# Performance work log

Measured on AMD Instinct MI355X. Metric: run time of the kernel, lower is better.

## Reference

```python
import jax, jax.numpy as jnp
import numpy as np

B, S, D, H = 2, 2048, 2048, 16
HD = D // H


def setup_inputs() -> dict:
    key = jax.random.key(0)
    ks = jax.random.split(key, 11)
    scale = 1.0 / np.sqrt(D)
    return {
        "query": jax.random.normal(ks[0], (B, S, D), jnp.float32),
        "key_": jax.random.normal(ks[1], (B, S, D), jnp.float32),
        "value": jax.random.normal(ks[2], (B, S, D), jnp.float32),
        "Wq": jax.random.normal(ks[3], (D, D), jnp.float32) * scale,
        "bq": jnp.zeros((D,), jnp.float32),
        "Wk": jax.random.normal(ks[4], (D, D), jnp.float32) * scale,
        "bk": jnp.zeros((D,), jnp.float32),
        "Wv": jax.random.normal(ks[5], (D, D), jnp.float32) * scale,
        "bv": jnp.zeros((D,), jnp.float32),
        "Wo": jax.random.normal(ks[6], (D, D), jnp.float32) * scale,
        "bo": jnp.zeros((D,), jnp.float32),
    }


def reference(query, key_, value, Wq, bq, Wk, bk, Wv, bv, Wo, bo):
    # Linear projections (torch Linear: x @ W.T + b)
    q = query @ Wq.T + bq   # [B,S,D]
    k = key_ @ Wk.T + bk
    v = value @ Wv.T + bv
    # split heads -> [B,H,S,HD]
    def split(x):
        return x.reshape(B, S, H, HD).transpose(0, 2, 1, 3)
    q, k, v = split(q), split(k), split(v)
    # scaled dot-product attention, full NxN softmax
    scores = jnp.einsum('bhqd,bhkd->bhqk', q, k) / jnp.sqrt(jnp.float32(HD))
    attn = jax.nn.softmax(scores, axis=-1)
    out = jnp.einsum('bhqk,bhkd->bhqd', attn, v)
    out = out.transpose(0, 2, 1, 3).reshape(B, S, D)
    return out @ Wo.T + bo
```

## Files before the change

kernel.cpp:

```cpp
#include <hip/hip_runtime.h>
#include <stdint.h>

#define B_  2
#define S_  2048
#define D_  2048
#define H_  16
#define HD_ 128
#define M_  (B_ * S_)

typedef unsigned short u16;
typedef __attribute__((ext_vector_type(8))) short bf16x8;
typedef __attribute__((ext_vector_type(4))) float f32x4;

__device__ __forceinline__ u16 f2bf(float f) {
  union { float f; unsigned u; } x; x.f = f;
  unsigned r = x.u + 0x7fffu + ((x.u >> 16) & 1u);
  return (u16)(r >> 16);
}
__device__ __forceinline__ void gload16(const void* g, void* l) {
  __builtin_amdgcn_global_load_lds(
      (const __attribute__((address_space(1))) void*)g,
      (__attribute__((address_space(3))) void*)l, 16, 0, 0);
}
__device__ __forceinline__ void store_out(u16* p, float v)  { *p = f2bf(v); }
__device__ __forceinline__ void store_out(float* p, float v){ *p = v; }

struct CvtArgs {
  const float* src[7];
  u16* dst[7];
  int n8[7];
};
__global__ void __launch_bounds__(256)
cvt_all(CvtArgs a) {
  const int seg = blockIdx.y;
  const float* __restrict__ src = a.src[seg];
  u16* __restrict__ dst = a.dst[seg];
  const int n8 = a.n8[seg];
  int idx = blockIdx.x * 256 + threadIdx.x;
  const int stride = gridDim.x * 256;
  for (int i = idx; i < n8; i += stride) {
    f32x4 x = ((const f32x4*)src)[2 * i];
    f32x4 y = ((const f32x4*)src)[2 * i + 1];
    bf16x8 o;
    o[0] = (short)f2bf(x[0]); o[1] = (short)f2bf(x[1]);
    o[2] = (short)f2bf(x[2]); o[3] = (short)f2bf(x[3]);
    o[4] = (short)f2bf(y[0]); o[5] = (short)f2bf(y[1]);
    o[6] = (short)f2bf(y[2]); o[7] = (short)f2bf(y[3]);
    ((bf16x8*)dst)[i] = o;
  }
}

template <typename OT, bool BM>
__global__ void __launch_bounds__(512, 2)
gemm_nt_bias(const u16* __restrict__ A, const u16* __restrict__ W,
             const float* __restrict__ bias, OT* __restrict__ C,
             int M, int N, int K, float oscale, int lognbx) {
  __shared__ u16 lds[3 * 24576];

  const int tid  = threadIdx.x;
  const int lane = tid & 63;
  const int wave = tid >> 6;
  const int wm = wave >> 1;
  const int wn = wave & 1;
  const int lr = lane & 15;
  const int lg = lane >> 4;

  const int bid = blockIdx.x;
  const int cpx = gridDim.x >> 3;
  const int swz = (bid & 7) * cpx + (bid >> 3);
  const int m0 = (swz & ((1 << lognbx) - 1)) << 8;
  const int n0 = (swz >> lognbx) << 7;

  const f32x4 zero4 = {0.f, 0.f, 0.f, 0.f};
  f32x4 acc[4][4];
#pragma unroll
  for (int i = 0; i < 4; i++)
#pragma unroll
    for (int j = 0; j < 4; j++) acc[i][j] = zero4;

  size_t aoff[4];
#pragma unroll
  for (int i = 0; i < 4; i++) {
    const int c = i * 512 + tid;
    const int row = c >> 3;
    const int cc = (c & 7) ^ (row & 7);
    aoff[i] = (size_t)(m0 + row) * K + cc * 8;
  }
  size_t boff[2];
#pragma unroll
  for (int i = 0; i < 2; i++) {
    const int c = i * 512 + tid;
    const int row = c >> 3;
    const int cc = (c & 7) ^ (row & 7);
    boff[i] = (size_t)(n0 + row) * K + cc * 8;
  }

  u16* b0 = lds;
  u16* b1 = lds + 24576;
  u16* b2 = lds + 49152;

#define STAGE(buf, t)                                                     \
  do {                                                                    \
    const int k0s = (t) * 64;                                             \
    gload16(A + aoff[0] + k0s, (buf) + tid * 8);                          \
    gload16(A + aoff[1] + k0s, (buf) + 4096 + tid * 8);                   \
    gload16(A + aoff[2] + k0s, (buf) + 8192 + tid * 8);                   \
    gload16(A + aoff[3] + k0s, (buf) + 12288 + tid * 8);                  \
    gload16(W + boff[0] + k0s, (buf) + 16384 + tid * 8);                  \
    gload16(W + boff[1] + k0s, (buf) + 20480 + tid * 8);                  \
  } while (0)

  const int nt = K >> 6;
  STAGE(b0, 0);
  STAGE(b1, 1);

  for (int t = 0; t < nt; ++t) {
    if (t + 1 < nt) {
      asm volatile("s_waitcnt vmcnt(6)" ::: "memory");
    } else {
      asm volatile("s_waitcnt vmcnt(0)" ::: "memory");
    }
    __builtin_amdgcn_sched_barrier(0);
    __builtin_amdgcn_s_barrier();

    if (t + 2 < nt) STAGE(b2, t + 2);

#pragma unroll
    for (int ks = 0; ks < 2; ks++) {
      bf16x8 af[4], bfv[4];
#pragma unroll
      for (int mi = 0; mi < 4; mi++) {
        const int row = wm * 64 + mi * 16 + lr;
        const int pos = (ks * 4 + lg) ^ (row & 7);
        af[mi] = *(const bf16x8*)&b0[row * 64 + pos * 8];
      }
#pragma unroll
      for (int ni = 0; ni < 4; ni++) {
        const int row = wn * 64 + ni * 16 + lr;
        const int pos = (ks * 4 + lg) ^ (row & 7);
        bfv[ni] = *(const bf16x8*)&b0[16384 + row * 64 + pos * 8];
      }
      __builtin_amdgcn_s_setprio(1);
#pragma unroll
      for (int mi = 0; mi < 4; mi++)
#pragma unroll
        for (int ni = 0; ni < 4; ni++)
          acc[mi][ni] = __builtin_amdgcn_mfma_f32_16x16x32_bf16(
              af[mi], bfv[ni], acc[mi][ni], 0, 0, 0);
      __builtin_amdgcn_s_setprio(0);
    }

    u16* tmp = b0; b0 = b1; b1 = b2; b2 = tmp;
  }
#undef STAGE

  const int rbase = (lane >> 4) * 4;
#pragma unroll
  for (int ni = 0; ni < 4; ni++) {
    const int n = n0 + wn * 64 + ni * 16 + lr;
    float bv = 0.f;
    if (!BM) bv = bias[n];
#pragma unroll
    for (int mi = 0; mi < 4; mi++) {
#pragma unroll
      for (int j = 0; j < 4; j++) {
        const int m = m0 + wm * 64 + mi * 16 + rbase + j;
        const float bm = BM ? bias[m] : bv;
        store_out(&C[(size_t)m * N + n], (acc[mi][ni][j] + bm) * oscale);
      }
    }
  }
}

__global__ void __launch_bounds__(512, 2)
gemm2_256(const u16* __restrict__ Aq, const u16* __restrict__ Wqw,
          const float* __restrict__ bqv, u16* __restrict__ Cq, float osq,
          const u16* __restrict__ Ak, const u16* __restrict__ Wkw,
          const float* __restrict__ bkv, u16* __restrict__ Ck) {
  __shared__ u16 lds[2 * 32768];

  const int job = blockIdx.x >> 7;
  const u16* __restrict__ A = job ? Ak : Aq;
  const u16* __restrict__ W = job ? Wkw : Wqw;
  const float* __restrict__ bias = job ? bkv : bqv;
  u16* __restrict__ C = job ? Ck : Cq;
  const float oscale = job ? 1.0f : osq;
  const int K = D_, N = D_;

  const int tid  = threadIdx.x;
  const int lane = tid & 63;
  const int wave = tid >> 6;
  const int wm = wave >> 2;
  const int wn = wave & 3;
  const int lr = lane & 15;
  const int lg = lane >> 4;

  const int lbid = blockIdx.x & 127;
  const int swz = (lbid & 7) * 16 + (lbid >> 3);
  const int m0 = (swz & 15) << 8;
  const int n0 = (swz >> 4) << 8;

  const f32x4 zero4 = {0.f, 0.f, 0.f, 0.f};
  f32x4 acc[8][4];
#pragma unroll
  for (int i = 0; i < 8; i++)
#pragma unroll
    for (int j = 0; j < 4; j++) acc[i][j] = zero4;

  size_t aoff[4], boff[4];
#pragma unroll
  for (int i = 0; i < 4; i++) {
    const int c = i * 512 + tid;
    const int row = c >> 3;
    const int cc = (c & 7) ^ (row & 7);
    aoff[i] = (size_t)(m0 + row) * K + cc * 8;
    boff[i] = (size_t)(n0 + row) * K + cc * 8;
  }

  u16* cur = lds;
  u16* nxt = lds + 32768;

#define STAGE2(buf, t)                                                    \
  do {                                                                    \
    const int k0s = (t) * 64;                                             \
    gload16(A + aoff[0] + k0s, (buf) + tid * 8);                          \
    gload16(A + aoff[1] + k0s, (buf) + 4096 + tid * 8);                   \
    gload16(A + aoff[2] + k0s, (buf) + 8192 + tid * 8);                   \
    gload16(A + aoff[3] + k0s, (buf) + 12288 + tid * 8);                  \
    gload16(W + boff[0] + k0s, (buf) + 16384 + tid * 8);                  \
    gload16(W + boff[1] + k0s, (buf) + 20480 + tid * 8);                  \
    gload16(W + boff[2] + k0s, (buf) + 24576 + tid * 8);                  \
    gload16(W + boff[3] + k0s, (buf) + 28672 + tid * 8);                  \
  } while (0)

  const int nt = K >> 6;
  STAGE2(cur, 0);

  for (int t = 0; t < nt; ++t) {
    asm volatile("s_waitcnt vmcnt(0)" ::: "memory");
    __builtin_amdgcn_sched_barrier(0);
    __builtin_amdgcn_s_barrier();

    if (t + 1 < nt) STAGE2(nxt, t + 1);

#pragma unroll
    for (int ks = 0; ks < 2; ks++) {
      bf16x8 af[8], bfv[4];
#pragma unroll
      for (int mi = 0; mi < 8; mi++) {
        const int row = wm * 128 + mi * 16 + lr;
        const int pos = (ks * 4 + lg) ^ (row & 7);
        af[mi] = *(const bf16x8*)&cur[row * 64 + pos * 8];
      }
#pragma unroll
      for (int ni = 0; ni < 4; ni++) {
        const int row = wn * 64 + ni * 16 + lr;
        const int pos = (ks * 4 + lg) ^ (row & 7);
        bfv[ni] = *(const bf16x8*)&cur[16384 + row * 64 + pos * 8];
      }
      __builtin_amdgcn_s_setprio(1);
#pragma unroll
      for (int mi = 0; mi < 8; mi++)
#pragma unroll
        for (int ni = 0; ni < 4; ni++)
          acc[mi][ni] = __builtin_amdgcn_mfma_f32_16x16x32_bf16(
              af[mi], bfv[ni], acc[mi][ni], 0, 0, 0);
      __builtin_amdgcn_s_setprio(0);
    }

    u16* tmp = cur; cur = nxt; nxt = tmp;
  }
#undef STAGE2

  const int rbase = (lane >> 4) * 4;
#pragma unroll
  for (int ni = 0; ni < 4; ni++) {
    const int n = n0 + wn * 64 + ni * 16 + lr;
    const float bv = bias[n];
#pragma unroll
    for (int mi = 0; mi < 8; mi++) {
#pragma unroll
      for (int j = 0; j < 4; j++) {
        const int m = m0 + wm * 128 + mi * 16 + rbase + j;
        C[(size_t)m * N + n] = f2bf((acc[mi][ni][j] + bv) * oscale);
      }
    }
  }
}

__global__ void __launch_bounds__(512)
flash_attn(const u16* __restrict__ Q, const u16* __restrict__ K,
           const u16* __restrict__ VT, u16* __restrict__ O) {
  __shared__ u16 Klds[64 * 128];
  __shared__ u16 VTlds[128 * 64];
  __shared__ u16 Plds[8][32 * 64];

  const int tid  = threadIdx.x;
  const int lane = tid & 63;
  const int wave = tid >> 6;
  const int lr = lane & 15;
  const int lk = (lane >> 4) * 8;
  const int rbase = (lane >> 4) * 4;

  const int bid = blockIdx.x;
  const int swz = (bid & 7) * 32 + (bid >> 3);
  const int qblk = swz & 7;
  const int bh   = swz >> 3;
  const int b = bh >> 4, h = bh & 15;
  const size_t base   = (size_t)b * S_ * D_ + (size_t)h * HD_;
  const size_t vtbase = (size_t)h * HD_ * M_ + (size_t)b * S_;
  const int q0 = qblk * 256 + wave * 32;

  bf16x8 qf[2][4];
#pragma unroll
  for (int qb = 0; qb < 2; qb++)
#pragma unroll
    for (int c = 0; c < 4; c++)
      qf[qb][c] = *(const bf16x8*)
          &Q[base + (size_t)(q0 + qb * 16 + lr) * D_ + c * 32 + lk];

  const f32x4 zero4 = {0.f, 0.f, 0.f, 0.f};
  f32x4 of[2][8];
#pragma unroll
  for (int qb = 0; qb < 2; qb++)
#pragma unroll
    for (int c = 0; c < 8; c++) of[qb][c] = zero4;
  float lrow[2][4] = {{0.f,0.f,0.f,0.f},{0.f,0.f,0.f,0.f}};

  const int kr0 = tid >> 4, kdc = (tid & 15) * 8;
  const int vr0 = tid >> 3, vsc = (tid & 7) * 8;

  bf16x8 kreg[2], vreg[2];
#pragma unroll
  for (int t = 0; t < 2; t++) {
    kreg[t] = *(const bf16x8*)&K[base + (size_t)(kr0 + 32 * t) * D_ + kdc];
    vreg[t] = *(const bf16x8*)&VT[vtbase + (size_t)(vr0 + 64 * t) * M_ + vsc];
  }

  for (int kb0 = 0; kb0 < S_; kb0 += 64) {
    __syncthreads();
#pragma unroll
    for (int t = 0; t < 2; t++) {
      const int krow = kr0 + 32 * t;
      *(bf16x8*)&Klds[krow * 128 + (kdc ^ ((krow & 7) << 3))] = kreg[t];
      const int vrow = vr0 + 64 * t;
      *(bf16x8*)&VTlds[vrow * 64 + (vsc ^ ((vrow & 7) << 3))] = vreg[t];
    }
    __syncthreads();

    if (kb0 + 64 < S_) {
      const int kn = kb0 + 64;
#pragma unroll
      for (int t = 0; t < 2; t++) {
        kreg[t] = *(const bf16x8*)&K[base + (size_t)(kn + kr0 + 32 * t) * D_ + kdc];
        vreg[t] = *(const bf16x8*)&VT[vtbase + (size_t)(vr0 + 64 * t) * M_ + kn + vsc];
      }
    }

    f32x4 s[2][4];
#pragma unroll
    for (int qb = 0; qb < 2; qb++)
#pragma unroll
      for (int kc = 0; kc < 4; kc++) s[qb][kc] = zero4;
    __builtin_amdgcn_s_setprio(1);
#pragma unroll
    for (int c = 0; c < 4; c++) {
#pragma unroll
      for (int kc = 0; kc < 4; kc++) {
        const int krow = kc * 16 + lr;
        bf16x8 kf = *(const bf16x8*)
            &Klds[krow * 128 + ((c * 32 + lk) ^ ((krow & 7) << 3))];
        s[0][kc] = __builtin_amdgcn_mfma_f32_16x16x32_bf16(qf[0][c], kf, s[0][kc], 0, 0, 0);
        s[1][kc] = __builtin_amdgcn_mfma_f32_16x16x32_bf16(qf[1][c], kf, s[1][kc], 0, 0, 0);
      }
    }
    __builtin_amdgcn_s_setprio(0);

#pragma unroll
    for (int qb = 0; qb < 2; qb++) {
#pragma unroll
      for (int j = 0; j < 4; j++) {
        float p0 = __builtin_amdgcn_exp2f(s[qb][0][j]);
        float p1 = __builtin_amdgcn_exp2f(s[qb][1][j]);
        float p2 = __builtin_amdgcn_exp2f(s[qb][2][j]);
        float p3 = __builtin_amdgcn_exp2f(s[qb][3][j]);
        lrow[qb][j] += (p0 + p1) + (p2 + p3);
        const int prow = qb * 16 + rbase + j;
        const int pb = prow * 64;
        const int sw = (prow & 7) << 3;
        Plds[wave][pb + ((     lr) ^ sw)] = f2bf(p0);
        Plds[wave][pb + ((16 + lr) ^ sw)] = f2bf(p1);
        Plds[wave][pb + ((32 + lr) ^ sw)] = f2bf(p2);
        Plds[wave][pb + ((48 + lr) ^ sw)] = f2bf(p3);
      }
    }

    __builtin_amdgcn_s_setprio(1);
#pragma unroll
    for (int h2 = 0; h2 < 2; h2++) {
      bf16x8 pa[2];
#pragma unroll
      for (int qb = 0; qb < 2; qb++) {
        const int prow = qb * 16 + lr;
        pa[qb] = *(const bf16x8*)
            &Plds[wave][prow * 64 + ((h2 * 32 + lk) ^ ((prow & 7) << 3))];
      }
#pragma unroll
      for (int c = 0; c < 8; c++) {
        const int vrow = c * 16 + lr;
        bf16x8 vf = *(const bf16x8*)
            &VTlds[vrow * 64 + ((h2 * 32 + lk) ^ ((vrow & 7) << 3))];
        of[0][c] = __builtin_amdgcn_mfma_f32_16x16x32_bf16(pa[0], vf, of[0][c], 0, 0, 0);
        of[1][c] = __builtin_amdgcn_mfma_f32_16x16x32_bf16(pa[1], vf, of[1][c], 0, 0, 0);
      }
    }
    __builtin_amdgcn_s_setprio(0);
  }

#pragma unroll
  for (int qb = 0; qb < 2; qb++) {
    float rinv[4];
#pragma unroll
    for (int j = 0; j < 4; j++) {
      float rs = lrow[qb][j];
      rs += __shfl_xor(rs, 1);
      rs += __shfl_xor(rs, 2);
      rs += __shfl_xor(rs, 4);
      rs += __shfl_xor(rs, 8);
      rinv[j] = 1.0f / rs;
    }
#pragma unroll
    for (int c = 0; c < 8; c++)
#pragma unroll
      for (int j = 0; j < 4; j++)
        O[base + (size_t)(q0 + qb * 16 + rbase + j) * D_ + c * 16 + lr] =
            f2bf(of[qb][c][j] * rinv[j]);
  }
}

extern "C" void kernel_launch(void* const* d_in, const int* in_sizes, int n_in,
                              void* d_out, int out_size, void* d_ws, size_t ws_size,
                              hipStream_t stream) {
  const float* query = (const float*)d_in[0];
  const float* key_  = (const float*)d_in[1];
  const float* value = (const float*)d_in[2];
  const float* Wq = (const float*)d_in[3];
  const float* bq = (const float*)d_in[4];
  const float* Wk = (const float*)d_in[5];
  const float* bk = (const float*)d_in[6];
  const float* Wv = (const float*)d_in[7];
  const float* bv = (const float*)d_in[8];
  const float* Wo = (const float*)d_in[9];
  const float* bo = (const float*)d_in[10];
  float* out = (float*)d_out;

  const size_t act = (size_t)M_ * D_;
  const size_t wsz = (size_t)D_ * D_;

  u16* p = (u16*)d_ws;
  u16* qb = p;  p += act;
  u16* kb = p;  p += act;
  u16* vb = p;  p += act;
  u16* wqb = p; p += wsz;
  u16* wkb = p; p += wsz;
  u16* wvb = p; p += wsz;
  u16* wob = p; p += wsz;
  u16* Qp  = p; p += act;
  u16* Kp  = p; p += act;
  u16* VpT = p; p += act;
  u16* AO  = p; p += act;

  dim3 blk(256);
  {
    CvtArgs a;
    a.src[0] = query; a.dst[0] = qb;  a.n8[0] = (int)(act / 8);
    a.src[1] = key_;  a.dst[1] = kb;  a.n8[1] = (int)(act / 8);
    a.src[2] = value; a.dst[2] = vb;  a.n8[2] = (int)(act / 8);
    a.src[3] = Wq;    a.dst[3] = wqb; a.n8[3] = (int)(wsz / 8);
    a.src[4] = Wk;    a.dst[4] = wkb; a.n8[4] = (int)(wsz / 8);
    a.src[5] = Wv;    a.dst[5] = wvb; a.n8[5] = (int)(wsz / 8);
    a.src[6] = Wo;    a.dst[6] = wob; a.n8[6] = (int)(wsz / 8);
    hipLaunchKernelGGL(cvt_all, dim3(512, 7), blk, 0, stream, a);
  }

  const float qscale = 1.4426950408889634f / 11.313708498984761f;

  dim3 g1(256);
  dim3 blk512(512);
  hipLaunchKernelGGL(gemm2_256, g1, blk512, 0, stream,
                     qb, wqb, bq, Qp, qscale,
                     kb, wkb, bk, Kp);
  hipLaunchKernelGGL((gemm_nt_bias<u16, true>), g1, blk512, 0, stream,
                     wvb, vb, bv, VpT, D_, M_, D_, 1.0f, 3);

  hipLaunchKernelGGL(flash_attn, dim3(256), blk512, 0, stream, Qp, Kp, VpT, AO);

  hipLaunchKernelGGL((gemm_nt_bias<float, false>), g1, blk512, 0, stream,
                     AO, wob, bo, out, M_, D_, D_, 1.0f, 4);
}
```

Baseline: 259.8 us.

## Triple-buffer K/V tiles in flash attention with direct global-to-LDS loads

Replaces the register-staged double-sync K/VT load in the attention loop with a three-stage ring of LDS buffers filled by global_load_lds, placing the swizzle on the global address side. Each iteration waits on vmcnt and issues a single barrier, prefetching two tiles ahead. The aim is to cut the per-tile register staging, the LDS store instructions and one barrier, and to hide global latency better. In exchange, LDS use grows to 96KB plus the P buffers, which may limit occupancy, and the correctness of the single-barrier reuse depends on the buffer rotation.

```diff
diff --git a/kernel.cpp b/kernel.cpp
--- a/kernel.cpp
+++ b/kernel.cpp
@@ -291,8 +291,7 @@
 __global__ void __launch_bounds__(512)
 flash_attn(const u16* __restrict__ Q, const u16* __restrict__ K,
            const u16* __restrict__ VT, u16* __restrict__ O) {
-  __shared__ u16 Klds[64 * 128];
-  __shared__ u16 VTlds[128 * 64];
+  __shared__ u16 kv[3 * 16384];
   __shared__ u16 Plds[8][32 * 64];
 
   const int tid  = threadIdx.x;
@@ -327,35 +326,42 @@
     for (int c = 0; c < 8; c++) of[qb][c] = zero4;
   float lrow[2][4] = {{0.f,0.f,0.f,0.f},{0.f,0.f,0.f,0.f}};
 
-  const int kr0 = tid >> 4, kdc = (tid & 15) * 8;
-  const int vr0 = tid >> 3, vsc = (tid & 7) * 8;
-
-  bf16x8 kreg[2], vreg[2];
-#pragma unroll
-  for (int t = 0; t < 2; t++) {
-    kreg[t] = *(const bf16x8*)&K[base + (size_t)(kr0 + 32 * t) * D_ + kdc];
-    vreg[t] = *(const bf16x8*)&VT[vtbase + (size_t)(vr0 + 64 * t) * M_ + vsc];
-  }
-
-  for (int kb0 = 0; kb0 < S_; kb0 += 64) {
-    __syncthreads();
-#pragma unroll
-    for (int t = 0; t < 2; t++) {
-      const int krow = kr0 + 32 * t;
-      *(bf16x8*)&Klds[krow * 128 + (kdc ^ ((krow & 7) << 3))] = kreg[t];
-      const int vrow = vr0 + 64 * t;
-      *(bf16x8*)&VTlds[vrow * 64 + (vsc ^ ((vrow & 7) << 3))] = vreg[t];
-    }
-    __syncthreads();
-
-    if (kb0 + 64 < S_) {
-      const int kn = kb0 + 64;
-#pragma unroll
-      for (int t = 0; t < 2; t++) {
-        kreg[t] = *(const bf16x8*)&K[base + (size_t)(kn + kr0 + 32 * t) * D_ + kdc];
-        vreg[t] = *(const bf16x8*)&VT[vtbase + (size_t)(vr0 + 64 * t) * M_ + kn + vsc];
-      }
-    }
+  const size_t ka0 = base + (size_t)(tid >> 4) * D_
+                   + (size_t)(((tid & 15) ^ ((tid >> 4) & 7)) * 8);
+  const size_t ka1 = ka0 + (size_t)32 * D_;
+  const size_t va0 = vtbase + (size_t)(tid >> 3) * M_
+                   + (size_t)(((tid & 7) ^ ((tid >> 3) & 7)) * 8);
+  const size_t va1 = va0 + (size_t)64 * M_;
+
+  u16* b0 = kv;
+  u16* b1 = kv + 16384;
+  u16* b2 = kv + 32768;
+
+#define FSTAGE(buf, kb)                                                   \
+  do {                                                                    \
+    gload16(K + ka0 + (size_t)(kb) * D_, (buf) + tid * 8);                \
+    gload16(K + ka1 + (size_t)(kb) * D_, (buf) + (tid + 512) * 8);        \
+    gload16(VT + va0 + (kb), (buf) + 8192 + tid * 8);                     \
+    gload16(VT + va1 + (kb), (buf) + 8192 + (tid + 512) * 8);             \
+  } while (0)
+
+  const int nt = S_ / 64;
+  FSTAGE(b0, 0);
+  FSTAGE(b1, 64);
+
+  for (int t = 0; t < nt; ++t) {
+    if (t + 1 < nt) {
+      asm volatile("s_waitcnt vmcnt(4)" ::: "memory");
+    } else {
+      asm volatile("s_waitcnt vmcnt(0)" ::: "memory");
+    }
+    __builtin_amdgcn_sched_barrier(0);
+    __builtin_amdgcn_s_barrier();
+
+    if (t + 2 < nt) FSTAGE(b2, (t + 2) * 64);
+
+    const u16* Kt  = b0;
+    const u16* VTt = b0 + 8192;
 
     f32x4 s[2][4];
 #pragma unroll
@@ -369,7 +375,7 @@
       for (int kc = 0; kc < 4; kc++) {
         const int krow = kc * 16 + lr;
         bf16x8 kf = *(const bf16x8*)
-            &Klds[krow * 128 + ((c * 32 + lk) ^ ((krow & 7) << 3))];
+            &Kt[krow * 128 + ((c * 32 + lk) ^ ((krow & 7) << 3))];
         s[0][kc] = __builtin_amdgcn_mfma_f32_16x16x32_bf16(qf[0][c], kf, s[0][kc], 0, 0, 0);
         s[1][kc] = __builtin_amdgcn_mfma_f32_16x16x32_bf16(qf[1][c], kf, s[1][kc], 0, 0, 0);
       }
@@ -409,13 +415,16 @@
       for (int c = 0; c < 8; c++) {
         const int vrow = c * 16 + lr;
         bf16x8 vf = *(const bf16x8*)
-            &VTlds[vrow * 64 + ((h2 * 32 + lk) ^ ((vrow & 7) << 3))];
+            &VTt[vrow * 64 + ((h2 * 32 + lk) ^ ((vrow & 7) << 3))];
         of[0][c] = __builtin_amdgcn_mfma_f32_16x16x32_bf16(pa[0], vf, of[0][c], 0, 0, 0);
         of[1][c] = __builtin_amdgcn_mfma_f32_16x16x32_bf16(pa[1], vf, of[1][c], 0, 0, 0);
       }
     }
     __builtin_amdgcn_s_setprio(0);
-  }
+
+    u16* tmp = b0; b0 = b1; b1 = b2; b2 = tmp;
+  }
+#undef FSTAGE
 
 #pragma unroll
   for (int qb = 0; qb < 2; qb++) {
```

Result: no change. 257.1 us, median of 3 (-1.0%).
